# Kernel optimization log

Measured on AMD Instinct MI355X. Metric: run time of the kernel, lower is better.

## Reference

```python
import jax, jax.numpy as jnp
import numpy as np

QK = 32  # GGML Q8_0 block size

def dequant_q8_0(w_q, w_scales):
    # w_q: [out, in] int8-valued quants; w_scales: [out, in//QK] per-block scales
    out_f, in_f = w_q.shape
    q = w_q.astype(w_scales.dtype).reshape(out_f, in_f // QK, QK)
    w = q * w_scales[:, :, None]  # broadcast scale over block
    return w.reshape(out_f, in_f)

def setup_inputs() -> dict:
    key = jax.random.key(0)
    k1, k2, k3, k4 = jax.random.split(key, 4)
    OUT, IN, TOK = 12288, 3072, 4096
    x = jax.random.normal(k1, (TOK, IN), dtype=jnp.float32)
    w_q = jax.random.randint(k2, (OUT, IN), -127, 128, dtype=jnp.int32)
    w_scales = jax.random.uniform(k3, (OUT, IN // QK), dtype=jnp.float32) * 0.01
    bias = jax.random.normal(k4, (OUT,), dtype=jnp.float32) * 0.01
    return {"x": x, "w_q": w_q, "w_scales": w_scales, "bias": bias}

def reference(x, w_q, w_scales, bias):
    # DequantingLinear.forward: dequantize weight (and bias) then F.linear
    weight = dequant_q8_0(w_q, w_scales)          # [OUT, IN]
    return x @ weight.T + bias                    # [TOK, OUT]
```

## Files before the change

### kernel.cpp

```cpp
#include <hip/hip_runtime.h>
#include <hip/hip_bf16.h>
#include <stdint.h>


typedef __bf16 bf16;
typedef __bf16 bf16x8 __attribute__((ext_vector_type(8)));
typedef float f32x4 __attribute__((ext_vector_type(4)));

#define AS1 __attribute__((address_space(1)))
#define AS3 __attribute__((address_space(3)))

__device__ __forceinline__ void gload_lds16(const void* g, void* l) {
    __builtin_amdgcn_global_load_lds((AS1 void*)g, (AS3 void*)l, 16, 0, 0);
}

#define MFMA16(d, x, y) d = __builtin_amdgcn_mfma_f32_16x16x32_bf16(x, y, d, 0, 0, 0)

__global__ __launch_bounds__(128) void k_dequant(
    const int* __restrict__ q, const float* __restrict__ sc,
    bf16* __restrict__ w, int IN) {
    const int row = blockIdx.y;
    const int k = (blockIdx.x * 128 + threadIdx.x) * 8;
    if (k >= IN) return;
    const float s = sc[(size_t)row * (IN >> 5) + (k >> 5)];
    const size_t base = (size_t)row * IN + k;
    const int4 q0 = *(const int4*)(q + base);
    const int4 q1 = *(const int4*)(q + base + 4);
    bf16x8 o;
    o[0] = (bf16)(q0.x * s); o[1] = (bf16)(q0.y * s);
    o[2] = (bf16)(q0.z * s); o[3] = (bf16)(q0.w * s);
    o[4] = (bf16)(q1.x * s); o[5] = (bf16)(q1.y * s);
    o[6] = (bf16)(q1.z * s); o[7] = (bf16)(q1.w * s);
    *(bf16x8*)(w + base) = o;
}

__global__ __launch_bounds__(256) void k_cvt(
    const float* __restrict__ x, bf16* __restrict__ xb, long long n8) {
    long long i = (long long)blockIdx.x * 256 + threadIdx.x;
    const long long stride = (long long)gridDim.x * 256;
    for (; i < n8; i += stride) {
        const float4 a = *(const float4*)(x + i * 8);
        const float4 b = *(const float4*)(x + i * 8 + 4);
        bf16x8 o;
        o[0] = (bf16)a.x; o[1] = (bf16)a.y; o[2] = (bf16)a.z; o[3] = (bf16)a.w;
        o[4] = (bf16)b.x; o[5] = (bf16)b.y; o[6] = (bf16)b.z; o[7] = (bf16)b.w;
        *(bf16x8*)(xb + i * 8) = o;
    }
}

__global__ __launch_bounds__(512, 2) void k_gemm8p(
    const bf16* __restrict__ A, const bf16* __restrict__ B,
    const float* __restrict__ bias, float* __restrict__ C,
    int M, int N, int K) {
    __shared__ __align__(16) char lds[131072];
    const int tid = threadIdx.x;
    const int wv = tid >> 6, ln = tid & 63;
    const int wm = wv >> 2, wn = wv & 3;
    const int nbn = N >> 8;
    const int nwg = gridDim.x;
    const int q8 = nwg >> 3, r8 = nwg & 7;
    const int xcd = blockIdx.x & 7, lin = blockIdx.x >> 3;
    const int swz = (xcd < r8 ? xcd * (q8 + 1)
                              : r8 * (q8 + 1) + (xcd - r8) * q8) + lin;
    const int bm = swz / nbn, bn = swz % nbn;

    const size_t rowb = (size_t)K * 2;
    const int L0 = tid, L1 = tid + 512;
    const int x0 = (L0 & 7) ^ ((L0 >> 3) & 7);
    const int x1 = (L1 & 7) ^ ((L1 >> 3) & 7);
    const int fr0 = ((L0 >> 3) << 1) | (x0 >> 2), c40 = x0 & 3;
    const int fr1 = ((L1 >> 3) << 1) | (x1 >> 2), c41 = x1 & 3;
    const char* Asrc0 = (const char*)A + ((size_t)(bm << 8) + fr0) * rowb + c40 * 16;
    const char* Asrc1 = (const char*)A + ((size_t)(bm << 8) + fr1) * rowb + c41 * 16;
    const char* Bsrc0 = (const char*)B + ((size_t)(bn << 8) + fr0) * rowb + c40 * 16;
    const char* Bsrc1 = (const char*)B + ((size_t)(bn << 8) + fr1) * rowb + c41 * 16;
    const int ldsw = wv << 10;

#define STG(bb_, uo_, kt_, P_) do {                                           \
        const size_t kb_ = (size_t)(kt_) << 1;                                \
        gload_lds16(P_##src0 + kb_, lds + (bb_) + (uo_) + ldsw);              \
        gload_lds16(P_##src1 + kb_, lds + (bb_) + (uo_) + 8192 + ldsw);       \
    } while (0)

    const int chunk = (((ln & 1) << 2) | (ln >> 4)) ^ ((ln >> 1) & 7);
    const int aoff = (wm << 13) + (((ln & 15) >> 1) << 7) + (chunk << 4);
    const int boff = (wn << 12) + (((ln & 15) >> 1) << 7) + (chunk << 4);

    f32x4 acc[8][4] = {};
    bf16x8 pb[4];

#define BAR __builtin_amdgcn_s_barrier()
#define VMW6 asm volatile("s_waitcnt vmcnt(6)" ::: "memory")
#define VMW0 asm volatile("s_waitcnt vmcnt(0)" ::: "memory")
#define NOST (void)0

#define PHASE(bb_, h_, ks_, RDB_, STAGE_STMT, ENDW_STMT) do {                 \
        const char* base_ = lds + (bb_) + (ks_) * 16384;                      \
        bf16x8 pa_[4];                                                        \
        _Pragma("unroll")                                                     \
        for (int m = 0; m < 4; ++m)                                           \
            pa_[m] = *(const bf16x8*)(base_ + ((h_) << 12) + aoff + (m << 10)); \
        if (RDB_) {                                                           \
            _Pragma("unroll")                                                 \
            for (int n = 0; n < 4; ++n)                                       \
                pb[n] = *(const bf16x8*)(base_ + 32768 + boff + (n << 10));   \
        }                                                                     \
        STAGE_STMT;                                                           \
        BAR;                                                                  \
        asm volatile("s_waitcnt lgkmcnt(0)" ::: "memory");                    \
        __builtin_amdgcn_s_setprio(1);                                        \
        _Pragma("unroll")                                                     \
        for (int m = 0; m < 4; ++m)                                           \
            _Pragma("unroll")                                                 \
            for (int n = 0; n < 4; ++n)                                       \
                MFMA16(acc[(h_) * 4 + m][n], pa_[m], pb[n]);                  \
        __builtin_amdgcn_s_setprio(0);                                        \
        ENDW_STMT;                                                            \
        BAR;                                                                  \
    } while (0)

    STG(0, 0,     0,  A);
    STG(0, 16384, 32, A);
    STG(0, 32768, 0,  B);
    STG(0, 49152, 32, B);
    STG(65536, 32768, 64, B);
    STG(65536, 0,     64, A);
    STG(65536, 49152, 96, B);
    VMW6;
    BAR;

    const int NI = K >> 7;
    for (int j = 0; j < NI - 1; ++j) {
        const int kO = (j << 7) + 64;
        const int kE = (j << 7) + 128;
        const int kN = (j << 7) + 192;
        PHASE(0,     0, 0, 1, STG(65536, 16384, kO + 32, A), NOST);
        PHASE(0,     1, 0, 0, STG(0,     32768, kE,      B), NOST);
        PHASE(0,     0, 1, 1, STG(0,     0,     kE,      A), NOST);
        PHASE(0,     1, 1, 0, STG(0,     49152, kE + 32, B), VMW6);
        PHASE(65536, 0, 0, 1, STG(0,     16384, kE + 32, A), NOST);
        PHASE(65536, 1, 0, 0, STG(65536, 32768, kN,      B), NOST);
        PHASE(65536, 0, 1, 1, STG(65536, 0,     kN,      A), NOST);
        PHASE(65536, 1, 1, 0, STG(65536, 49152, kN + 32, B), VMW6);
    }
    {
        const int kO = ((NI - 1) << 7) + 64;
        PHASE(0,     0, 0, 1, STG(65536, 16384, kO + 32, A), NOST);
        PHASE(0,     1, 0, 0, NOST,                          NOST);
        PHASE(0,     0, 1, 1, NOST,                          NOST);
        PHASE(0,     1, 1, 0, NOST,                          VMW0);
        PHASE(65536, 0, 0, 1, NOST,                          NOST);
        PHASE(65536, 1, 0, 0, NOST,                          NOST);
        PHASE(65536, 0, 1, 1, NOST,                          NOST);
        PHASE(65536, 1, 1, 0, NOST,                          NOST);
    }
#undef PHASE
#undef STG

    const int erow = (bm << 8) + (wm << 7) + ((ln >> 4) << 2);
    const int ecol = (bn << 8) + (wn << 6) + (ln & 15);
    float bv[4];
#pragma unroll
    for (int n = 0; n < 4; ++n) bv[n] = bias[ecol + (n << 4)];
#pragma unroll
    for (int m = 0; m < 8; ++m)
#pragma unroll
        for (int r = 0; r < 4; ++r) {
            float* Crow = C + (size_t)(erow + (m << 4) + r) * N + ecol;
#pragma unroll
            for (int n = 0; n < 4; ++n)
                Crow[n << 4] = acc[m][n][r] + bv[n];
        }
}

__global__ __launch_bounds__(256) void k_fused(
    const float* __restrict__ X, const int* __restrict__ Q,
    const float* __restrict__ SC, const float* __restrict__ bias,
    float* __restrict__ C, int M, int N, int K) {
    __shared__ __align__(16) bf16 sA[128 * 32];
    __shared__ __align__(16) bf16 sB[128 * 32];
    const int tid = threadIdx.x;
    const int wv = tid >> 6;
    const int ln = tid & 63;
    const int nbn = N >> 7;
    const int nwg = gridDim.x;
    const int q8 = nwg >> 3, r8 = nwg & 7;
    const int xcd = blockIdx.x & 7, lin = blockIdx.x >> 3;
    const int swz = (xcd < r8 ? xcd * (q8 + 1)
                              : r8 * (q8 + 1) + (xcd - r8) * q8) + lin;
    const int bm = swz / nbn, bn = swz % nbn;
    const int wr = (wv >> 1) << 6;
    const int wc = (wv & 1) << 6;
    const int srow = tid >> 1;
    const int sk = (tid & 1) << 4;

    f32x4 acc[4][4] = {};
    const float* xrow = X + (size_t)((bm << 7) + srow) * K + sk;
    const int* qrow = Q + (size_t)((bn << 7) + srow) * K + sk;
    const float* scrow = SC + (size_t)((bn << 7) + srow) * (K >> 5);

    for (int kt = 0; kt < K; kt += 32) {
        const float4 a0 = *(const float4*)(xrow + kt);
        const float4 a1 = *(const float4*)(xrow + kt + 4);
        const float4 a2 = *(const float4*)(xrow + kt + 8);
        const float4 a3 = *(const float4*)(xrow + kt + 12);
        const int4 q0 = *(const int4*)(qrow + kt);
        const int4 q1 = *(const int4*)(qrow + kt + 4);
        const int4 q2 = *(const int4*)(qrow + kt + 8);
        const int4 q3 = *(const int4*)(qrow + kt + 12);
        const float s = scrow[(kt + sk) >> 5];
        bf16x8 wa0, wa1, wb0, wb1;
        wa0[0] = (bf16)a0.x; wa0[1] = (bf16)a0.y; wa0[2] = (bf16)a0.z; wa0[3] = (bf16)a0.w;
        wa0[4] = (bf16)a1.x; wa0[5] = (bf16)a1.y; wa0[6] = (bf16)a1.z; wa0[7] = (bf16)a1.w;
        wa1[0] = (bf16)a2.x; wa1[1] = (bf16)a2.y; wa1[2] = (bf16)a2.z; wa1[3] = (bf16)a2.w;
        wa1[4] = (bf16)a3.x; wa1[5] = (bf16)a3.y; wa1[6] = (bf16)a3.z; wa1[7] = (bf16)a3.w;
        wb0[0] = (bf16)(q0.x * s); wb0[1] = (bf16)(q0.y * s);
        wb0[2] = (bf16)(q0.z * s); wb0[3] = (bf16)(q0.w * s);
        wb0[4] = (bf16)(q1.x * s); wb0[5] = (bf16)(q1.y * s);
        wb0[6] = (bf16)(q1.z * s); wb0[7] = (bf16)(q1.w * s);
        wb1[0] = (bf16)(q2.x * s); wb1[1] = (bf16)(q2.y * s);
        wb1[2] = (bf16)(q2.z * s); wb1[3] = (bf16)(q2.w * s);
        wb1[4] = (bf16)(q3.x * s); wb1[5] = (bf16)(q3.y * s);
        wb1[6] = (bf16)(q3.z * s); wb1[7] = (bf16)(q3.w * s);
        __syncthreads();
        *(bf16x8*)(sA + srow * 32 + sk) = wa0;
        *(bf16x8*)(sA + srow * 32 + sk + 8) = wa1;
        *(bf16x8*)(sB + srow * 32 + sk) = wb0;
        *(bf16x8*)(sB + srow * 32 + sk + 8) = wb1;
        __syncthreads();

        bf16x8 af[4], bg[4];
#pragma unroll
        for (int m = 0; m < 4; ++m)
            af[m] = *(const bf16x8*)(sA + ((wr + (m << 4) + (ln & 15)) << 5) +
                                     ((ln >> 4) << 3));
#pragma unroll
        for (int n = 0; n < 4; ++n)
            bg[n] = *(const bf16x8*)(sB + ((wc + (n << 4) + (ln & 15)) << 5) +
                                     ((ln >> 4) << 3));
#pragma unroll
        for (int m = 0; m < 4; ++m)
#pragma unroll
            for (int n = 0; n < 4; ++n)
                acc[m][n] = __builtin_amdgcn_mfma_f32_16x16x32_bf16(
                    af[m], bg[n], acc[m][n], 0, 0, 0);
    }

    float bv[4];
#pragma unroll
    for (int n = 0; n < 4; ++n)
        bv[n] = bias[(bn << 7) + wc + (n << 4) + (ln & 15)];
#pragma unroll
    for (int m = 0; m < 4; ++m) {
        const int grow0 = (bm << 7) + wr + (m << 4) + ((ln >> 4) << 2);
#pragma unroll
        for (int r = 0; r < 4; ++r) {
            float* Crow = C + (size_t)(grow0 + r) * N;
#pragma unroll
            for (int n = 0; n < 4; ++n)
                Crow[(bn << 7) + wc + (n << 4) + (ln & 15)] =
                    acc[m][n][r] + bv[n];
        }
    }
}

extern "C" void kernel_launch(void* const* d_in, const int* in_sizes, int n_in,
                              void* d_out, int out_size, void* d_ws, size_t ws_size,
                              hipStream_t stream) {
    const float* x = (const float*)d_in[0];
    const int* wq = (const int*)d_in[1];
    const float* sc = (const float*)d_in[2];
    const float* bias = (const float*)d_in[3];
    float* out = (float*)d_out;

    const long long xN = in_sizes[0];
    const long long wN = in_sizes[1];
    const int OUT = in_sizes[3];
    const int IN = (int)(wN / OUT);
    const int TOK = (int)(xN / IN);
    const int M = TOK, N = OUT, K = IN;

    const size_t wb_bytes = (size_t)wN * 2;
    const size_t xb_bytes = (size_t)xN * 2;
    const bool ok8p = (M % 256 == 0) && (N % 256 == 0) && (K % 128 == 0) &&
                      (K >= 256);

    if (ok8p && ws_size >= wb_bytes + xb_bytes) {
        bf16* Wb = (bf16*)d_ws;
        bf16* Xb = (bf16*)((char*)d_ws + wb_bytes);
        dim3 dq_grid((IN / 8 + 127) / 128, OUT);
        k_dequant<<<dq_grid, 128, 0, stream>>>(wq, sc, Wb, IN);
        const long long n8 = xN / 8;
        int cvt_blocks = (int)((n8 + 255) / 256);
        if (cvt_blocks > 2048) cvt_blocks = 2048;
        k_cvt<<<cvt_blocks, 256, 0, stream>>>(x, Xb, n8);
        const int grid = (M / 256) * (N / 256);
        k_gemm8p<<<grid, 512, 0, stream>>>(Xb, Wb, bias, out, M, N, K);
    } else {
        const int grid = (M / 128) * (N / 128);
        k_fused<<<grid, 256, 0, stream>>>(x, wq, sc, bias, out, M, N, K);
    }
}
```

Baseline: 342.8 us.

## Double-buffer LDS fragment registers to overlap reads with MFMA in GEMM loop

Restructures the GEMM main loop so LDS fragment reads for the next phase are issued into a second register set while MFMAs run on the current one. This removes the per-phase lgkmcnt(0) wait and one barrier per phase. Global-load wait counts and stage ordering are adjusted to match. It uses more VGPRs for the extra fragment buffers and needs careful barrier placement to avoid LDS races.

Result: no change. 340.8 us (-0.6%).

```diff
diff --git a/kernel.cpp b/kernel.cpp
--- a/kernel.cpp
+++ b/kernel.cpp
@@ -87,75 +87,72 @@
     const int boff = (wn << 12) + (((ln & 15) >> 1) << 7) + (chunk << 4);
 
     f32x4 acc[8][4] = {};
-    bf16x8 pb[4];
+    bf16x8 pa0[4], pa1[4], pb0[4], pb1[4];
+
+#define RDA4(PA_, bb_, ks_, h_) do { _Pragma("unroll")                        \
+        for (int m = 0; m < 4; ++m)                                           \
+            PA_[m] = *(const bf16x8*)(lds + (bb_) + (ks_) * 16384 +           \
+                                      ((h_) << 12) + aoff + (m << 10));       \
+    } while (0)
+#define RDB4(PB_, bb_, ks_) do { _Pragma("unroll")                            \
+        for (int n = 0; n < 4; ++n)                                           \
+            PB_[n] = *(const bf16x8*)(lds + (bb_) + (ks_) * 16384 + 32768 +   \
+                                      boff + (n << 10));                      \
+    } while (0)
+#define MF(h_, PA_, PB_) do {                                                 \
+        __builtin_amdgcn_s_setprio(1);                                        \
+        _Pragma("unroll") for (int m = 0; m < 4; ++m)                         \
+        _Pragma("unroll") for (int n = 0; n < 4; ++n)                         \
+            MFMA16(acc[(h_) * 4 + m][n], PA_[m], PB_[n]);                     \
+        __builtin_amdgcn_s_setprio(0);                                        \
+    } while (0)
 
 #define BAR __builtin_amdgcn_s_barrier()
-#define VMW6 asm volatile("s_waitcnt vmcnt(6)" ::: "memory")
+#define VMW8 asm volatile("s_waitcnt vmcnt(8)" ::: "memory")
+#define VMW4 asm volatile("s_waitcnt vmcnt(4)" ::: "memory")
+#define VMW10 asm volatile("s_waitcnt vmcnt(10)" ::: "memory")
 #define VMW0 asm volatile("s_waitcnt vmcnt(0)" ::: "memory")
-#define NOST (void)0
-
-#define PHASE(bb_, h_, ks_, RDB_, STAGE_STMT, ENDW_STMT) do {                 \
-        const char* base_ = lds + (bb_) + (ks_) * 16384;                      \
-        bf16x8 pa_[4];                                                        \
-        _Pragma("unroll")                                                     \
-        for (int m = 0; m < 4; ++m)                                           \
-            pa_[m] = *(const bf16x8*)(base_ + ((h_) << 12) + aoff + (m << 10)); \
-        if (RDB_) {                                                           \
-            _Pragma("unroll")                                                 \
-            for (int n = 0; n < 4; ++n)                                       \
-                pb[n] = *(const bf16x8*)(base_ + 32768 + boff + (n << 10));   \
-        }                                                                     \
-        STAGE_STMT;                                                           \
-        BAR;                                                                  \
-        asm volatile("s_waitcnt lgkmcnt(0)" ::: "memory");                    \
-        __builtin_amdgcn_s_setprio(1);                                        \
-        _Pragma("unroll")                                                     \
-        for (int m = 0; m < 4; ++m)                                           \
-            _Pragma("unroll")                                                 \
-            for (int n = 0; n < 4; ++n)                                       \
-                MFMA16(acc[(h_) * 4 + m][n], pa_[m], pb[n]);                  \
-        __builtin_amdgcn_s_setprio(0);                                        \
-        ENDW_STMT;                                                            \
-        BAR;                                                                  \
-    } while (0)
 
     STG(0, 0,     0,  A);
-    STG(0, 16384, 32, A);
     STG(0, 32768, 0,  B);
     STG(0, 49152, 32, B);
+    STG(0, 16384, 32, A);
     STG(65536, 32768, 64, B);
     STG(65536, 0,     64, A);
     STG(65536, 49152, 96, B);
-    VMW6;
+    VMW10;
     BAR;
+    RDA4(pa0, 0, 0, 0);
+    RDB4(pb0, 0, 0);
 
     const int NI = K >> 7;
+#pragma unroll 1
     for (int j = 0; j < NI - 1; ++j) {
-        const int kO = (j << 7) + 64;
-        const int kE = (j << 7) + 128;
-        const int kN = (j << 7) + 192;
-        PHASE(0,     0, 0, 1, STG(65536, 16384, kO + 32, A), NOST);
-        PHASE(0,     1, 0, 0, STG(0,     32768, kE,      B), NOST);
-        PHASE(0,     0, 1, 1, STG(0,     0,     kE,      A), NOST);
-        PHASE(0,     1, 1, 0, STG(0,     49152, kE + 32, B), VMW6);
-        PHASE(65536, 0, 0, 1, STG(0,     16384, kE + 32, A), NOST);
-        PHASE(65536, 1, 0, 0, STG(65536, 32768, kN,      B), NOST);
-        PHASE(65536, 0, 1, 1, STG(65536, 0,     kN,      A), NOST);
-        PHASE(65536, 1, 1, 0, STG(65536, 49152, kN + 32, B), VMW6);
+        const int kO = (j << 7) + 64, kE2 = kO + 64, kO2 = kE2 + 64;
+        BAR;  RDA4(pa1, 0, 0, 1);                      STG(65536, 16384, kO + 32, A);  MF(0, pa0, pb0);
+        VMW8; BAR; RDA4(pa0, 0, 1, 0); RDB4(pb1, 0, 1); STG(0, 32768, kE2, B);         MF(1, pa1, pb0);
+        BAR;  RDA4(pa1, 0, 1, 1);                      STG(0, 0, kE2, A);              MF(0, pa0, pb1);
+        VMW8; BAR; RDA4(pa0, 65536, 0, 0); RDB4(pb0, 65536, 0); STG(0, 49152, kE2 + 32, B); MF(1, pa1, pb1);
+        BAR;  RDA4(pa1, 65536, 0, 1);                  STG(0, 16384, kE2 + 32, A);     MF(0, pa0, pb0);
+        VMW8; BAR; RDA4(pa0, 65536, 1, 0); RDB4(pb1, 65536, 1); STG(65536, 32768, kO2, B); MF(1, pa1, pb0);
+        BAR;  RDA4(pa1, 65536, 1, 1);                  STG(65536, 0, kO2, A);          MF(0, pa0, pb1);
+        VMW8; BAR; RDA4(pa0, 0, 0, 0); RDB4(pb0, 0, 0); STG(65536, 49152, kO2 + 32, B); MF(1, pa1, pb1);
     }
     {
         const int kO = ((NI - 1) << 7) + 64;
-        PHASE(0,     0, 0, 1, STG(65536, 16384, kO + 32, A), NOST);
-        PHASE(0,     1, 0, 0, NOST,                          NOST);
-        PHASE(0,     0, 1, 1, NOST,                          NOST);
-        PHASE(0,     1, 1, 0, NOST,                          VMW0);
-        PHASE(65536, 0, 0, 1, NOST,                          NOST);
-        PHASE(65536, 1, 0, 0, NOST,                          NOST);
-        PHASE(65536, 0, 1, 1, NOST,                          NOST);
-        PHASE(65536, 1, 1, 0, NOST,                          NOST);
-    }
-#undef PHASE
+        BAR;  RDA4(pa1, 0, 0, 1);                      STG(65536, 16384, kO + 32, A);  MF(0, pa0, pb0);
+        VMW8; BAR; RDA4(pa0, 0, 1, 0); RDB4(pb1, 0, 1);                                MF(1, pa1, pb0);
+        BAR;  RDA4(pa1, 0, 1, 1);                                                     MF(0, pa0, pb1);
+        VMW4; BAR; RDA4(pa0, 65536, 0, 0); RDB4(pb0, 65536, 0);                        MF(1, pa1, pb1);
+        BAR;  RDA4(pa1, 65536, 0, 1);                                                 MF(0, pa0, pb0);
+        VMW0; BAR; RDA4(pa0, 65536, 1, 0); RDB4(pb1, 65536, 1);                        MF(1, pa1, pb0);
+        BAR;  RDA4(pa1, 65536, 1, 1);                                                 MF(0, pa0, pb1);
+        BAR;                                                                          MF(1, pa1, pb1);
+    }
 #undef STG
+#undef RDA4
+#undef RDB4
+#undef MF
 
     const int erow = (bm << 8) + (wm << 7) + ((ln >> 4) << 2);
     const int ecol = (bn << 8) + (wn << 6) + (ln & 15);
```

## Replace 256x256 eight-phase GEMM with 256x128 double-buffered tile kernel

Applied to the files above, without the earlier changes.

Swaps the 256x256 output-tile GEMM, which used 128KB of LDS and an eight-phase pipeline with partial vmcnt waits, for a 256x128 tile that uses 48KB of LDS and a simple two-stage double buffer. The launch bound asks for 4 workgroups per CU, aiming for higher occupancy and more latency hiding through co-resident blocks instead of deep in-block prefetch. The cost is lower arithmetic intensity per tile: more reloads of A across tiles and half the accumulators per wave. A full vmcnt(0) wait every K-step also reduces overlap between loads and compute.

New measurement: 383.9 us. 12.0% more time.

```diff
diff --git a/kernel.cpp b/kernel.cpp
--- a/kernel.cpp
+++ b/kernel.cpp
@@ -48,15 +48,15 @@
     }
 }
 
-__global__ __launch_bounds__(512, 2) void k_gemm8p(
+__global__ __launch_bounds__(512, 4) void k_gemm2b(
     const bf16* __restrict__ A, const bf16* __restrict__ B,
     const float* __restrict__ bias, float* __restrict__ C,
     int M, int N, int K) {
-    __shared__ __align__(16) char lds[131072];
+    __shared__ __align__(16) char lds[49152];
     const int tid = threadIdx.x;
     const int wv = tid >> 6, ln = tid & 63;
-    const int wm = wv >> 2, wn = wv & 3;
-    const int nbn = N >> 8;
+    const int wm = wv >> 1, wn = wv & 1;
+    const int nbn = N >> 7;
     const int nwg = gridDim.x;
     const int q8 = nwg >> 3, r8 = nwg & 7;
     const int xcd = blockIdx.x & 7, lin = blockIdx.x >> 3;
@@ -72,98 +72,81 @@
     const int fr1 = ((L1 >> 3) << 1) | (x1 >> 2), c41 = x1 & 3;
     const char* Asrc0 = (const char*)A + ((size_t)(bm << 8) + fr0) * rowb + c40 * 16;
     const char* Asrc1 = (const char*)A + ((size_t)(bm << 8) + fr1) * rowb + c41 * 16;
-    const char* Bsrc0 = (const char*)B + ((size_t)(bn << 8) + fr0) * rowb + c40 * 16;
-    const char* Bsrc1 = (const char*)B + ((size_t)(bn << 8) + fr1) * rowb + c41 * 16;
+    const char* Bsrc0 = (const char*)B + ((size_t)(bn << 7) + fr0) * rowb + c40 * 16;
     const int ldsw = wv << 10;
 
-#define STG(bb_, uo_, kt_, P_) do {                                           \
+#define STGA(bb_, kt_) do {                                                   \
         const size_t kb_ = (size_t)(kt_) << 1;                                \
-        gload_lds16(P_##src0 + kb_, lds + (bb_) + (uo_) + ldsw);              \
-        gload_lds16(P_##src1 + kb_, lds + (bb_) + (uo_) + 8192 + ldsw);       \
+        gload_lds16(Asrc0 + kb_, lds + (bb_) + ldsw);                         \
+        gload_lds16(Asrc1 + kb_, lds + (bb_) + 8192 + ldsw);                  \
     } while (0)
+#define STGB(bb_, kt_) do {                                                   \
+        const size_t kb_ = (size_t)(kt_) << 1;                                \
+        gload_lds16(Bsrc0 + kb_, lds + (bb_) + 16384 + ldsw);                 \
+    } while (0)
 
     const int chunk = (((ln & 1) << 2) | (ln >> 4)) ^ ((ln >> 1) & 7);
-    const int aoff = (wm << 13) + (((ln & 15) >> 1) << 7) + (chunk << 4);
-    const int boff = (wn << 12) + (((ln & 15) >> 1) << 7) + (chunk << 4);
-
-    f32x4 acc[8][4] = {};
-    bf16x8 pb[4];
+    const int aoff = (wm << 12) + (((ln & 15) >> 1) << 7) + (chunk << 4);
+    const int boff = 16384 + (wn << 12) + (((ln & 15) >> 1) << 7) + (chunk << 4);
+
+    f32x4 acc[4][4] = {};
 
 #define BAR __builtin_amdgcn_s_barrier()
-#define VMW6 asm volatile("s_waitcnt vmcnt(6)" ::: "memory")
 #define VMW0 asm volatile("s_waitcnt vmcnt(0)" ::: "memory")
-#define NOST (void)0
-
-#define PHASE(bb_, h_, ks_, RDB_, STAGE_STMT, ENDW_STMT) do {                 \
-        const char* base_ = lds + (bb_) + (ks_) * 16384;                      \
-        bf16x8 pa_[4];                                                        \
+#define LGK0 do { asm volatile("s_waitcnt lgkmcnt(0)" ::: "memory");          \
+                  __builtin_amdgcn_sched_barrier(0); } while (0)
+
+#define PHASE(rb_, STAGE_STMT, ENDW_STMT) do {                                \
+        bf16x8 pa_[4], pb_[4];                                                \
         _Pragma("unroll")                                                     \
         for (int m = 0; m < 4; ++m)                                           \
-            pa_[m] = *(const bf16x8*)(base_ + ((h_) << 12) + aoff + (m << 10)); \
-        if (RDB_) {                                                           \
-            _Pragma("unroll")                                                 \
-            for (int n = 0; n < 4; ++n)                                       \
-                pb[n] = *(const bf16x8*)(base_ + 32768 + boff + (n << 10));   \
-        }                                                                     \
+            pa_[m] = *(const bf16x8*)(lds + (rb_) + aoff + (m << 10));        \
+        _Pragma("unroll")                                                     \
+        for (int n = 0; n < 4; ++n)                                           \
+            pb_[n] = *(const bf16x8*)(lds + (rb_) + boff + (n << 10));        \
         STAGE_STMT;                                                           \
         BAR;                                                                  \
-        asm volatile("s_waitcnt lgkmcnt(0)" ::: "memory");                    \
+        LGK0;                                                                 \
         __builtin_amdgcn_s_setprio(1);                                        \
         _Pragma("unroll")                                                     \
         for (int m = 0; m < 4; ++m)                                           \
             _Pragma("unroll")                                                 \
             for (int n = 0; n < 4; ++n)                                       \
-                MFMA16(acc[(h_) * 4 + m][n], pa_[m], pb[n]);                  \
+                MFMA16(acc[m][n], pa_[m], pb_[n]);                            \
         __builtin_amdgcn_s_setprio(0);                                        \
         ENDW_STMT;                                                            \
         BAR;                                                                  \
     } while (0)
 
-    STG(0, 0,     0,  A);
-    STG(0, 16384, 32, A);
-    STG(0, 32768, 0,  B);
-    STG(0, 49152, 32, B);
-    STG(65536, 32768, 64, B);
-    STG(65536, 0,     64, A);
-    STG(65536, 49152, 96, B);
-    VMW6;
+    STGA(0, 0);
+    STGB(0, 0);
+    VMW0;
     BAR;
 
-    const int NI = K >> 7;
+    const int NT = K >> 5;
+    const int NI = NT >> 1;
+#pragma unroll 1
     for (int j = 0; j < NI - 1; ++j) {
-        const int kO = (j << 7) + 64;
-        const int kE = (j << 7) + 128;
-        const int kN = (j << 7) + 192;
-        PHASE(0,     0, 0, 1, STG(65536, 16384, kO + 32, A), NOST);
-        PHASE(0,     1, 0, 0, STG(0,     32768, kE,      B), NOST);
-        PHASE(0,     0, 1, 1, STG(0,     0,     kE,      A), NOST);
-        PHASE(0,     1, 1, 0, STG(0,     49152, kE + 32, B), VMW6);
-        PHASE(65536, 0, 0, 1, STG(0,     16384, kE + 32, A), NOST);
-        PHASE(65536, 1, 0, 0, STG(65536, 32768, kN,      B), NOST);
-        PHASE(65536, 0, 1, 1, STG(65536, 0,     kN,      A), NOST);
-        PHASE(65536, 1, 1, 0, STG(65536, 49152, kN + 32, B), VMW6);
+        const int k1 = (j << 6) + 32, k2 = k1 + 32;
+        PHASE(0,     { STGA(24576, k1); STGB(24576, k1); }, VMW0);
+        PHASE(24576, { STGA(0,     k2); STGB(0,     k2); }, VMW0);
     }
     {
-        const int kO = ((NI - 1) << 7) + 64;
-        PHASE(0,     0, 0, 1, STG(65536, 16384, kO + 32, A), NOST);
-        PHASE(0,     1, 0, 0, NOST,                          NOST);
-        PHASE(0,     0, 1, 1, NOST,                          NOST);
-        PHASE(0,     1, 1, 0, NOST,                          VMW0);
-        PHASE(65536, 0, 0, 1, NOST,                          NOST);
-        PHASE(65536, 1, 0, 0, NOST,                          NOST);
-        PHASE(65536, 0, 1, 1, NOST,                          NOST);
-        PHASE(65536, 1, 1, 0, NOST,                          NOST);
+        const int k1 = ((NI - 1) << 6) + 32;
+        PHASE(0,     { STGA(24576, k1); STGB(24576, k1); }, VMW0);
+        PHASE(24576, (void)0, (void)0);
     }
 #undef PHASE
-#undef STG
-
-    const int erow = (bm << 8) + (wm << 7) + ((ln >> 4) << 2);
-    const int ecol = (bn << 8) + (wn << 6) + (ln & 15);
+#undef STGA
+#undef STGB
+
+    const int erow = (bm << 8) + (wm << 6) + ((ln >> 4) << 2);
+    const int ecol = (bn << 7) + (wn << 6) + (ln & 15);
     float bv[4];
 #pragma unroll
     for (int n = 0; n < 4; ++n) bv[n] = bias[ecol + (n << 4)];
 #pragma unroll
-    for (int m = 0; m < 8; ++m)
+    for (int m = 0; m < 4; ++m)
 #pragma unroll
         for (int r = 0; r < 4; ++r) {
             float* Crow = C + (size_t)(erow + (m << 4) + r) * N + ecol;
@@ -282,10 +265,10 @@
 
     const size_t wb_bytes = (size_t)wN * 2;
     const size_t xb_bytes = (size_t)xN * 2;
-    const bool ok8p = (M % 256 == 0) && (N % 256 == 0) && (K % 128 == 0) &&
-                      (K >= 256);
-
-    if (ok8p && ws_size >= wb_bytes + xb_bytes) {
+    const bool ok2b = (M % 256 == 0) && (N % 128 == 0) && (K % 64 == 0) &&
+                      (K >= 64);
+
+    if (ok2b && ws_size >= wb_bytes + xb_bytes) {
         bf16* Wb = (bf16*)d_ws;
         bf16* Xb = (bf16*)((char*)d_ws + wb_bytes);
         dim3 dq_grid((IN / 8 + 127) / 128, OUT);
@@ -294,8 +277,8 @@
         int cvt_blocks = (int)((n8 + 255) / 256);
         if (cvt_blocks > 2048) cvt_blocks = 2048;
         k_cvt<<<cvt_blocks, 256, 0, stream>>>(x, Xb, n8);
-        const int grid = (M / 256) * (N / 256);
-        k_gemm8p<<<grid, 512, 0, stream>>>(Xb, Wb, bias, out, M, N, K);
+        const int grid = (M / 256) * (N / 128);
+        k_gemm2b<<<grid, 512, 0, stream>>>(Xb, Wb, bias, out, M, N, K);
     } else {
         const int grid = (M / 128) * (N / 128);
         k_fused<<<grid, 256, 0, stream>>>(x, wq, sc, bias, out, M, N, K);
```

## Halve per-phase barriers in pipelined bf16 GEMM main loop

Applied to the files above, without the earlier changes.

The per-phase macro drops its trailing barrier, so each compute phase has a single barrier. The global-load wait now comes before that barrier, so staged LDS data is complete before any wave reads it. A sched_barrier pins the MFMA block after the LDS wait, the main loop is marked not-unrolled, and the initial prefetch order is interleaved A/B. The goal is less barrier stall time between MFMA phases; the risk is an LDS write-after-read hazard if a wave's staging overlaps reads that other waves have not yet finished.

Result: no change. 336.4 us (-1.9%).

```diff
diff --git a/kernel.cpp b/kernel.cpp
--- a/kernel.cpp
+++ b/kernel.cpp
@@ -87,42 +87,42 @@
     const int boff = (wn << 12) + (((ln & 15) >> 1) << 7) + (chunk << 4);
 
     f32x4 acc[8][4] = {};
-    bf16x8 pb[4];
+    bf16x8 pa[4], pb[4];
 
 #define BAR __builtin_amdgcn_s_barrier()
 #define VMW6 asm volatile("s_waitcnt vmcnt(6)" ::: "memory")
 #define VMW0 asm volatile("s_waitcnt vmcnt(0)" ::: "memory")
-#define NOST (void)0
-
-#define PHASE(bb_, h_, ks_, RDB_, STAGE_STMT, ENDW_STMT) do {                 \
-        const char* base_ = lds + (bb_) + (ks_) * 16384;                      \
-        bf16x8 pa_[4];                                                        \
+#define NOP0 (void)0
+
+#define PH(bb_, ks_, h_, RDB_, STAGE_STMT, WAIT_STMT) do {                    \
         _Pragma("unroll")                                                     \
         for (int m = 0; m < 4; ++m)                                           \
-            pa_[m] = *(const bf16x8*)(base_ + ((h_) << 12) + aoff + (m << 10)); \
+            pa[m] = *(const bf16x8*)(lds + (bb_) + (ks_) * 16384 +            \
+                                     ((h_) << 12) + aoff + (m << 10));        \
         if (RDB_) {                                                           \
             _Pragma("unroll")                                                 \
             for (int n = 0; n < 4; ++n)                                       \
-                pb[n] = *(const bf16x8*)(base_ + 32768 + boff + (n << 10));   \
+                pb[n] = *(const bf16x8*)(lds + (bb_) + (ks_) * 16384 + 32768  \
+                                         + boff + (n << 10));                 \
         }                                                                     \
         STAGE_STMT;                                                           \
+        WAIT_STMT;                                                            \
         BAR;                                                                  \
         asm volatile("s_waitcnt lgkmcnt(0)" ::: "memory");                    \
+        __builtin_amdgcn_sched_barrier(0);                                    \
         __builtin_amdgcn_s_setprio(1);                                        \
         _Pragma("unroll")                                                     \
         for (int m = 0; m < 4; ++m)                                           \
             _Pragma("unroll")                                                 \
             for (int n = 0; n < 4; ++n)                                       \
-                MFMA16(acc[(h_) * 4 + m][n], pa_[m], pb[n]);                  \
+                MFMA16(acc[(h_) * 4 + m][n], pa[m], pb[n]);                   \
         __builtin_amdgcn_s_setprio(0);                                        \
-        ENDW_STMT;                                                            \
-        BAR;                                                                  \
     } while (0)
 
-    STG(0, 0,     0,  A);
-    STG(0, 16384, 32, A);
-    STG(0, 32768, 0,  B);
-    STG(0, 49152, 32, B);
+    STG(0,     0,     0,  A);
+    STG(0,     32768, 0,  B);
+    STG(0,     16384, 32, A);
+    STG(0,     49152, 32, B);
     STG(65536, 32768, 64, B);
     STG(65536, 0,     64, A);
     STG(65536, 49152, 96, B);
@@ -130,31 +130,32 @@
     BAR;
 
     const int NI = K >> 7;
+#pragma unroll 1
     for (int j = 0; j < NI - 1; ++j) {
-        const int kO = (j << 7) + 64;
-        const int kE = (j << 7) + 128;
-        const int kN = (j << 7) + 192;
-        PHASE(0,     0, 0, 1, STG(65536, 16384, kO + 32, A), NOST);
-        PHASE(0,     1, 0, 0, STG(0,     32768, kE,      B), NOST);
-        PHASE(0,     0, 1, 1, STG(0,     0,     kE,      A), NOST);
-        PHASE(0,     1, 1, 0, STG(0,     49152, kE + 32, B), VMW6);
-        PHASE(65536, 0, 0, 1, STG(0,     16384, kE + 32, A), NOST);
-        PHASE(65536, 1, 0, 0, STG(65536, 32768, kN,      B), NOST);
-        PHASE(65536, 0, 1, 1, STG(65536, 0,     kN,      A), NOST);
-        PHASE(65536, 1, 1, 0, STG(65536, 49152, kN + 32, B), VMW6);
+        const int kO1 = (j << 7) + 96;
+        const int kE2 = (j << 7) + 128;
+        const int kO2 = (j << 7) + 192;
+        PH(0,     0, 0, 1, STG(65536, 16384, kO1,      A), NOP0);
+        PH(0,     0, 1, 0, STG(0,     32768, kE2,      B), NOP0);
+        PH(0,     1, 0, 1, STG(0,     0,     kE2,      A), NOP0);
+        PH(0,     1, 1, 0, STG(0,     49152, kE2 + 32, B), VMW6);
+        PH(65536, 0, 0, 1, STG(0,     16384, kE2 + 32, A), NOP0);
+        PH(65536, 0, 1, 0, STG(65536, 32768, kO2,      B), NOP0);
+        PH(65536, 1, 0, 1, STG(65536, 0,     kO2,      A), NOP0);
+        PH(65536, 1, 1, 0, STG(65536, 49152, kO2 + 32, B), VMW6);
     }
     {
-        const int kO = ((NI - 1) << 7) + 64;
-        PHASE(0,     0, 0, 1, STG(65536, 16384, kO + 32, A), NOST);
-        PHASE(0,     1, 0, 0, NOST,                          NOST);
-        PHASE(0,     0, 1, 1, NOST,                          NOST);
-        PHASE(0,     1, 1, 0, NOST,                          VMW0);
-        PHASE(65536, 0, 0, 1, NOST,                          NOST);
-        PHASE(65536, 1, 0, 0, NOST,                          NOST);
-        PHASE(65536, 0, 1, 1, NOST,                          NOST);
-        PHASE(65536, 1, 1, 0, NOST,                          NOST);
-    }
-#undef PHASE
+        const int kO1 = ((NI - 1) << 7) + 96;
+        PH(0,     0, 0, 1, STG(65536, 16384, kO1, A), NOP0);
+        PH(0,     0, 1, 0, NOP0,                      NOP0);
+        PH(0,     1, 0, 1, NOP0,                      NOP0);
+        PH(0,     1, 1, 0, NOP0,                      VMW0);
+        PH(65536, 0, 0, 1, NOP0,                      NOP0);
+        PH(65536, 0, 1, 0, NOP0,                      NOP0);
+        PH(65536, 1, 0, 1, NOP0,                      NOP0);
+        PH(65536, 1, 1, 0, NOP0,                      NOP0);
+    }
+#undef PH
 #undef STG
 
     const int erow = (bm << 8) + (wm << 7) + ((ln >> 4) << 2);
```
